# Kernel tuning notes

Measured on AMD Instinct MI355X. Metric: run time of the kernel, lower is better.

## Reference

```python
import jax, jax.numpy as jnp
import numpy as np

EPS = 1.1920929e-07  # torch fp32 finfo eps used by F.rms_norm default

def rms_norm(x):
    return x * jax.lax.rsqrt(jnp.mean(jnp.square(x), axis=-1, keepdims=True) + EPS)

def setup_inputs() -> dict:
    key = jax.random.key(0)
    kx, kfc, kpr, krt = jax.random.split(key, 4)
    B, T, C, F = 4, 2048, 2048, 8192
    s = (3.0 ** 0.5) * C ** -0.5  # init scale used in init_weights
    x = jax.random.normal(kx, (B, T, C), dtype=jnp.float32)
    w_fc = jax.random.normal(kfc, (F, C), dtype=jnp.float32) * s
    w_proj = jax.random.normal(kpr, (C, F), dtype=jnp.float32) * (s * 0.1)
    w_router = jax.random.normal(krt, (1, C), dtype=jnp.float32) * 0.01  # router init std=0.01
    return {"x": x, "w_fc": w_fc, "w_proj": w_proj, "w_router": w_router}

def reference(x, w_fc, w_proj, w_router):
    # Router: (B,T,C) @ (C,1) -> (B,T) logits; STE mask (~0 or ~1 floats)
    logits = jnp.einsum('btc,oc->bto', x, w_router)[..., 0]  # (B,T)
    prob = jax.nn.sigmoid(logits)
    hard = (prob > 0.5).astype(x.dtype)
    mask_i = hard + prob - jax.lax.stop_gradient(prob)  # straight-through
    mask_bool = mask_i > 0.5  # (B,T)

    # Gated MLP (mixture-of-depth). The torch code gathers selected tokens,
    # runs the MLP on the compacted set, scatters into zeros, and multiplies
    # by mask_i. Mathematically identical dense form (honoring the mask):
    h = jnp.einsum('btc,fc->btf', rms_norm(x), w_fc)
    h = jnp.square(jax.nn.relu(h))  # relu(x)^2 activation
    mlp_out = jnp.einsum('btf,cf->btc', h, w_proj)
    gated = jnp.where(mask_bool[..., None], mlp_out * mask_i[..., None], 0.0)
    return x + gated
```

## Files before the change

### kernel.cpp

```cpp
#include <hip/hip_runtime.h>
#include <type_traits>
#include <utility>
#include <stdint.h>
#include <stddef.h>

#define TOKENS 8192
#define CDIM 2048
#define FDIM 8192
#define EPSV 1.1920929e-07f

typedef __attribute__((ext_vector_type(8))) short short8;
typedef __attribute__((ext_vector_type(8))) __bf16 bf16x8;
typedef __attribute__((ext_vector_type(4))) float floatx4;

template <typename V, typename = void> struct CanMfma : std::false_type {};
template <typename V>
struct CanMfma<V, std::void_t<decltype(__builtin_amdgcn_mfma_f32_16x16x32_bf16(
    std::declval<V>(), std::declval<V>(), std::declval<floatx4>(), 0, 0, 0))>>
    : std::true_type {};
using frag_t = std::conditional_t<CanMfma<short8>::value, short8, bf16x8>;

__device__ __forceinline__ floatx4 mfma_bf16(frag_t a, frag_t b, floatx4 c) {
    return __builtin_amdgcn_mfma_f32_16x16x32_bf16(a, b, c, 0, 0, 0);
}

__device__ __forceinline__ unsigned short f2bf(float f) {
    unsigned int u = __float_as_uint(f);
    u += 0x7fffu + ((u >> 16) & 1u);
    return (unsigned short)(u >> 16);
}

__global__ void zero_kernel(int* p) { if (threadIdx.x == 0) *p = 0; }

__global__ __launch_bounds__(256) void cvt2_kernel(
    const float* __restrict__ s1, unsigned short* __restrict__ d1, int n1,
    const float* __restrict__ s2, unsigned short* __restrict__ d2, int n2)
{
    int i = blockIdx.x * 256 + threadIdx.x;
    const float4* s; ushort4* d;
    if (i < n1) { s = (const float4*)s1; d = (ushort4*)d1; }
    else if (i < n1 + n2) { s = (const float4*)s2; d = (ushort4*)d2; i -= n1; }
    else return;
    float4 v = s[i];
    ushort4 o;
    o.x = f2bf(v.x); o.y = f2bf(v.y); o.z = f2bf(v.z); o.w = f2bf(v.w);
    d[i] = o;
}

__global__ __launch_bounds__(256) void router_kernel(
    const float* __restrict__ x, const float* __restrict__ wr,
    float* __restrict__ out, unsigned short* __restrict__ Xn,
    int* __restrict__ idx, float* __restrict__ mv, int* __restrict__ cnt)
{
    const int token = blockIdx.x;
    const int tid = threadIdx.x;
    const float4* xr = (const float4*)(x + (size_t)token * CDIM);
    const float4* w4 = (const float4*)wr;
    float4 a0 = xr[tid];
    float4 a1 = xr[tid + 256];
    float4 b0 = w4[tid];
    float4 b1 = w4[tid + 256];
    float ss = a0.x*a0.x + a0.y*a0.y + a0.z*a0.z + a0.w*a0.w
             + a1.x*a1.x + a1.y*a1.y + a1.z*a1.z + a1.w*a1.w;
    float dt = a0.x*b0.x + a0.y*b0.y + a0.z*b0.z + a0.w*b0.w
             + a1.x*b1.x + a1.y*b1.y + a1.z*b1.z + a1.w*b1.w;
    #pragma unroll
    for (int off = 32; off > 0; off >>= 1) {
        ss += __shfl_down(ss, off);
        dt += __shfl_down(dt, off);
    }
    __shared__ float red_ss[4], red_dt[4];
    __shared__ float s_rms;
    __shared__ int s_pos;
    const int wave = tid >> 6;
    if ((tid & 63) == 0) { red_ss[wave] = ss; red_dt[wave] = dt; }
    __syncthreads();
    if (tid == 0) {
        float S = red_ss[0] + red_ss[1] + red_ss[2] + red_ss[3];
        float D = red_dt[0] + red_dt[1] + red_dt[2] + red_dt[3];
        float prob = 1.0f / (1.0f + expf(-D));
        s_rms = 1.0f / sqrtf(S * (1.0f / (float)CDIM) + EPSV);
        int pos = -1;
        if (prob > 0.5f) {
            pos = atomicAdd(cnt, 1);
            idx[pos] = token;
            mv[pos] = (1.0f + prob) - prob;
        }
        s_pos = pos;
    }
    __syncthreads();
    float4* op = (float4*)(out + (size_t)token * CDIM);
    op[tid] = a0;
    op[tid + 256] = a1;
    const float rms = s_rms;
    const int pos = s_pos;
    if (pos >= 0) {
        ushort4* xp = (ushort4*)(Xn + (size_t)pos * CDIM);
        ushort4 o;
        o.x = f2bf(a0.x * rms); o.y = f2bf(a0.y * rms); o.z = f2bf(a0.z * rms); o.w = f2bf(a0.w * rms);
        xp[tid] = o;
        o.x = f2bf(a1.x * rms); o.y = f2bf(a1.y * rms); o.z = f2bf(a1.z * rms); o.w = f2bf(a1.w * rms);
        xp[tid + 256] = o;
    }
}

template <int K, int MODE, int LDO, int KSPLIT>
__global__ __launch_bounds__(256) void gemm_bt(
    const unsigned short* __restrict__ A,
    const unsigned short* __restrict__ B,
    unsigned short* __restrict__ Hout,
    float* __restrict__ out,
    const int* __restrict__ idx,
    const float* __restrict__ mv,
    const int* __restrict__ cntp)
{
    const int cnt = *cntp;
    const int bid = blockIdx.y * 64 + blockIdx.x;
    const int s = bid >> 6;
    const int w = bid & 63;
    const int mi = (s & 7) * 8 + (w & 7);
    const int ni = (s >> 3) * 8 + (w >> 3);
    const int m0 = mi * 128;
    if (m0 >= cnt) return;
    const int n0 = ni * 128;
    const int k0 = (int)blockIdx.z * (K / KSPLIT);

    __shared__ alignas(16) unsigned short lA[128 * 64];
    __shared__ alignas(16) unsigned short lB[128 * 64];

    const int tid = threadIdx.x;
    const int wave = tid >> 6;
    const int lane = tid & 63;
    const int wm = (wave >> 1) * 64;
    const int wn = (wave & 1) * 64;
    const int quad = lane >> 4;
    const int l16 = lane & 15;

    const int srow = lane >> 3;
    const int schunk = (lane & 7) ^ srow;

    const unsigned short* ap[4];
    const unsigned short* bp[4];
    #pragma unroll
    for (int p = 0; p < 4; ++p) {
        const int r = p * 32 + wave * 8 + srow;
        ap[p] = A + (size_t)(m0 + r) * K + k0 + schunk * 8;
        bp[p] = B + (size_t)(n0 + r) * K + k0 + schunk * 8;
    }

    floatx4 acc[4][4] = {};

    for (int kt = 0; kt < K / (64 * KSPLIT); ++kt) {
        #pragma unroll
        for (int p = 0; p < 4; ++p) {
            __builtin_amdgcn_global_load_lds(
                (__attribute__((address_space(1))) void*)ap[p],
                (__attribute__((address_space(3))) void*)&lA[(p * 32 + wave * 8) * 64],
                16, 0, 0);
            __builtin_amdgcn_global_load_lds(
                (__attribute__((address_space(1))) void*)bp[p],
                (__attribute__((address_space(3))) void*)&lB[(p * 32 + wave * 8) * 64],
                16, 0, 0);
            ap[p] += 64;
            bp[p] += 64;
        }
        __syncthreads();
        #pragma unroll
        for (int st = 0; st < 2; ++st) {
            frag_t af[4], bfv[4];
            #pragma unroll
            for (int t = 0; t < 4; ++t) {
                const int ra = wm + t * 16 + l16;
                const int ca = ((st * 4 + quad) ^ (ra & 7)) * 8;
                af[t] = *(const frag_t*)&lA[ra * 64 + ca];
                const int rb = wn + t * 16 + l16;
                const int cb = ((st * 4 + quad) ^ (rb & 7)) * 8;
                bfv[t] = *(const frag_t*)&lB[rb * 64 + cb];
            }
            #pragma unroll
            for (int tm = 0; tm < 4; ++tm)
                #pragma unroll
                for (int tn = 0; tn < 4; ++tn)
                    acc[tm][tn] = mfma_bf16(af[tm], bfv[tn], acc[tm][tn]);
        }
        __syncthreads();
    }

    if (MODE == 1) {
        #pragma unroll
        for (int tm = 0; tm < 4; ++tm) {
            const int gm = m0 + wm + tm * 16 + quad * 4;
            #pragma unroll
            for (int tn = 0; tn < 4; ++tn) {
                const int gn = n0 + wn + tn * 16 + l16;
                #pragma unroll
                for (int v = 0; v < 4; ++v) {
                    float h = fmaxf(acc[tm][tn][v], 0.0f);
                    Hout[(size_t)(gm + v) * LDO + gn] = f2bf(h * h);
                }
            }
        }
    } else {
        #pragma unroll
        for (int tm = 0; tm < 4; ++tm) {
            const int gmb = m0 + wm + tm * 16 + quad * 4;
            #pragma unroll
            for (int v = 0; v < 4; ++v) {
                const int gm = gmb + v;
                if (gm < cnt) {
                    const int token = idx[gm];
                    const float scale = mv[gm];
                    #pragma unroll
                    for (int tn = 0; tn < 4; ++tn) {
                        const int gn = n0 + wn + tn * 16 + l16;
                        atomicAdd(&out[(size_t)token * LDO + gn], scale * acc[tm][tn][v]);
                    }
                }
            }
        }
    }
}

extern "C" void kernel_launch(void* const* d_in, const int* in_sizes, int n_in,
                              void* d_out, int out_size, void* d_ws, size_t ws_size,
                              hipStream_t stream)
{
    const float* x   = (const float*)d_in[0];
    const float* wfc = (const float*)d_in[1];
    const float* wpr = (const float*)d_in[2];
    const float* wrt = (const float*)d_in[3];
    float* out = (float*)d_out;

    char* ws = (char*)d_ws;
    int*   cnt = (int*)ws;
    int*   idx = (int*)(ws + 256);
    float* mv  = (float*)(ws + 256 + 32768);
    unsigned short* Xn  = (unsigned short*)(ws + 65792);
    unsigned short* Wfc = (unsigned short*)(ws + 65792 + 33554432ULL);
    unsigned short* Wpr = (unsigned short*)(ws + 65792 + 67108864ULL);
    unsigned short* H   = (unsigned short*)(ws + 65792 + 100663296ULL);

    const int n4 = FDIM * CDIM / 4;
    zero_kernel<<<1, 64, 0, stream>>>(cnt);
    cvt2_kernel<<<(2 * n4 + 255) / 256, 256, 0, stream>>>(wfc, Wfc, n4, wpr, Wpr, n4);
    router_kernel<<<TOKENS, 256, 0, stream>>>(x, wrt, out, Xn, idx, mv, cnt);
    gemm_bt<CDIM, 1, FDIM, 1><<<dim3(64, FDIM / 128), 256, 0, stream>>>(
        Xn, Wfc, H, nullptr, nullptr, nullptr, cnt);
    gemm_bt<FDIM, 2, CDIM, 2><<<dim3(64, CDIM / 128, 2), 256, 0, stream>>>(
        H, Wpr, nullptr, out, idx, mv, cnt);
}
```

Baseline: 704.9 us.

## Double-buffer LDS tiles to overlap global loads with MFMA compute

Splits the LDS A/B tiles into two buffers and prefetches the next K-tile with global_load_lds while the current tile is consumed. Partial vmcnt waits and raw s_barrier replace the two __syncthreads per iteration. All fragments are loaded into registers before a barrier so the MFMAs run while the next tile lands. LDS use doubles to 64KB per block, which may reduce occupancy, and holding all fragments raises register pressure.

```diff
diff --git a/kernel.cpp b/kernel.cpp
--- a/kernel.cpp
+++ b/kernel.cpp
@@ -125,8 +125,8 @@
     const int n0 = ni * 128;
     const int k0 = (int)blockIdx.z * (K / KSPLIT);
 
-    __shared__ alignas(16) unsigned short lA[128 * 64];
-    __shared__ alignas(16) unsigned short lB[128 * 64];
+    __shared__ alignas(16) unsigned short lA[2][128 * 64];
+    __shared__ alignas(16) unsigned short lB[2][128 * 64];
 
     const int tid = threadIdx.x;
     const int wave = tid >> 6;
@@ -138,6 +138,7 @@
 
     const int srow = lane >> 3;
     const int schunk = (lane & 7) ^ srow;
+    const int ldsoff = (wave * 8) * 64;
 
     const unsigned short* ap[4];
     const unsigned short* bp[4];
@@ -149,41 +150,66 @@
     }
 
     floatx4 acc[4][4] = {};
-
-    for (int kt = 0; kt < K / (64 * KSPLIT); ++kt) {
-        #pragma unroll
-        for (int p = 0; p < 4; ++p) {
-            __builtin_amdgcn_global_load_lds(
-                (__attribute__((address_space(1))) void*)ap[p],
-                (__attribute__((address_space(3))) void*)&lA[(p * 32 + wave * 8) * 64],
-                16, 0, 0);
-            __builtin_amdgcn_global_load_lds(
-                (__attribute__((address_space(1))) void*)bp[p],
-                (__attribute__((address_space(3))) void*)&lB[(p * 32 + wave * 8) * 64],
-                16, 0, 0);
-            ap[p] += 64;
-            bp[p] += 64;
-        }
-        __syncthreads();
+    const int KT = K / (64 * KSPLIT);
+
+    #pragma unroll
+    for (int p = 0; p < 4; ++p) {
+        __builtin_amdgcn_global_load_lds(
+            (__attribute__((address_space(1))) void*)ap[p],
+            (__attribute__((address_space(3))) void*)&lA[0][p * 32 * 64 + ldsoff],
+            16, 0, 0);
+        __builtin_amdgcn_global_load_lds(
+            (__attribute__((address_space(1))) void*)bp[p],
+            (__attribute__((address_space(3))) void*)&lB[0][p * 32 * 64 + ldsoff],
+            16, 0, 0);
+        ap[p] += 64;
+        bp[p] += 64;
+    }
+
+    for (int kt = 0; kt < KT; ++kt) {
+        const int cur = kt & 1;
+        if (kt + 1 < KT) {
+            const int nb = cur ^ 1;
+            #pragma unroll
+            for (int p = 0; p < 4; ++p) {
+                __builtin_amdgcn_global_load_lds(
+                    (__attribute__((address_space(1))) void*)ap[p],
+                    (__attribute__((address_space(3))) void*)&lA[nb][p * 32 * 64 + ldsoff],
+                    16, 0, 0);
+                __builtin_amdgcn_global_load_lds(
+                    (__attribute__((address_space(1))) void*)bp[p],
+                    (__attribute__((address_space(3))) void*)&lB[nb][p * 32 * 64 + ldsoff],
+                    16, 0, 0);
+                ap[p] += 64;
+                bp[p] += 64;
+            }
+            asm volatile("s_waitcnt vmcnt(8)\n\ts_barrier" ::: "memory");
+        } else {
+            asm volatile("s_waitcnt vmcnt(0)\n\ts_barrier" ::: "memory");
+        }
+
+        frag_t af[2][4], bfv[2][4];
         #pragma unroll
         for (int st = 0; st < 2; ++st) {
-            frag_t af[4], bfv[4];
             #pragma unroll
             for (int t = 0; t < 4; ++t) {
                 const int ra = wm + t * 16 + l16;
                 const int ca = ((st * 4 + quad) ^ (ra & 7)) * 8;
-                af[t] = *(const frag_t*)&lA[ra * 64 + ca];
+                af[st][t] = *(const frag_t*)&lA[cur][ra * 64 + ca];
                 const int rb = wn + t * 16 + l16;
                 const int cb = ((st * 4 + quad) ^ (rb & 7)) * 8;
-                bfv[t] = *(const frag_t*)&lB[rb * 64 + cb];
-            }
+                bfv[st][t] = *(const frag_t*)&lB[cur][rb * 64 + cb];
+            }
+        }
+        asm volatile("s_waitcnt lgkmcnt(0)\n\ts_barrier" ::: "memory");
+
+        #pragma unroll
+        for (int st = 0; st < 2; ++st)
             #pragma unroll
             for (int tm = 0; tm < 4; ++tm)
                 #pragma unroll
                 for (int tn = 0; tn < 4; ++tn)
-                    acc[tm][tn] = mfma_bf16(af[tm], bfv[tn], acc[tm][tn]);
-        }
-        __syncthreads();
+                    acc[tm][tn] = mfma_bf16(af[st][tm], bfv[st][tn], acc[tm][tn]);
     }
 
     if (MODE == 1) {
```

Measured after the change: 756.4 us. +7.3%, slower.
